# Optimization experiments

Measured on AMD Instinct MI355X. Metric: run time of the kernel, lower is better.

## Reference

```python
import jax, jax.numpy as jnp
import numpy as np

N, B, SD, ED = 2048, 64, 512, 512


def setup_inputs() -> dict:
    key = jax.random.key(0)
    k1, k2, k3 = jax.random.split(key, 3)
    state_tm1 = jax.random.normal(k1, (B, SD), dtype=jnp.float32)
    embeddings = jax.random.normal(k2, (N, B, ED), dtype=jnp.float32)
    W = jax.random.normal(k3, (SD + ED, 1), dtype=jnp.float32) * 0.02
    b = jnp.zeros((1,), dtype=jnp.float32)
    return {"state_tm1": state_tm1, "embeddings": embeddings, "W": W, "b": b}


def reference(state_tm1, embeddings, W, b):
    # fc(concat(state, emb)) == state @ W_s + emb @ W_e + b  (split the weight)
    sd = state_tm1.shape[1]
    W_s, W_e = W[:sd], W[sd:]                      # [SD,1], [ED,1]
    state_score = state_tm1 @ W_s + b              # [B,1]
    logits = jnp.einsum('nbe,eo->nbo', embeddings, W_e) + state_score  # [N,B,1]
    alphas = jax.nn.softmax(logits, axis=0)        # softmax over items (dim 0)
    # weighted sum over items: [B, ED]
    return jnp.einsum('nbo,nbe->be', alphas, embeddings)
```

## Files before the change

kernel.cpp:

```cpp
#include <hip/hip_runtime.h>
#include <math.h>

#define BCOL 64
#define ED 512
#define NROWS 2048

__global__ void attn_partial_kernel(const float* __restrict__ emb,
                                    const float* __restrict__ W,
                                    float* __restrict__ accbuf,
                                    float* __restrict__ mbuf,
                                    float* __restrict__ lbuf,
                                    int G, int rowsPerWave)
{
    const int tid  = threadIdx.x;
    const int lane = tid & 63;
    const int wv   = tid >> 6;
    const int blk  = blockIdx.x;
    const int col  = blk % BCOL;
    const int chunk = blk / BCOL;
    const int g = chunk * 4 + wv;
    const int n0 = g * rowsPerWave;

    const float4* We4 = (const float4*)(W + 512);
    const float4 w0 = We4[lane];
    const float4 w1 = We4[lane + 64];

    float m = -INFINITY, l = 0.0f;
    float4 acc0 = {0.f, 0.f, 0.f, 0.f};
    float4 acc1 = {0.f, 0.f, 0.f, 0.f};

    const float4* row = (const float4*)(emb + ((size_t)n0 * BCOL + col) * ED);
    float4 a0 = row[lane];
    float4 a1 = row[lane + 64];

    for (int i = 0; i < rowsPerWave; ++i) {
        float4 b0, b1;
        if (i + 1 < rowsPerWave) {
            const float4* nrow =
                (const float4*)(emb + ((size_t)(n0 + i + 1) * BCOL + col) * ED);
            b0 = nrow[lane];
            b1 = nrow[lane + 64];
        }
        float p = a0.x * w0.x + a0.y * w0.y + a0.z * w0.z + a0.w * w0.w
                + a1.x * w1.x + a1.y * w1.y + a1.z * w1.z + a1.w * w1.w;
        #pragma unroll
        for (int off = 32; off > 0; off >>= 1)
            p += __shfl_xor(p, off, 64);
        const float s = p;

        const float mn   = fmaxf(m, s);
        const float corr = __expf(m - mn);
        const float pe   = __expf(s - mn);
        l = l * corr + pe;
        acc0.x = acc0.x * corr + pe * a0.x;
        acc0.y = acc0.y * corr + pe * a0.y;
        acc0.z = acc0.z * corr + pe * a0.z;
        acc0.w = acc0.w * corr + pe * a0.w;
        acc1.x = acc1.x * corr + pe * a1.x;
        acc1.y = acc1.y * corr + pe * a1.y;
        acc1.z = acc1.z * corr + pe * a1.z;
        acc1.w = acc1.w * corr + pe * a1.w;
        m = mn;

        a0 = b0;
        a1 = b1;
    }

    float4* out4 = (float4*)(accbuf + ((size_t)col * G + g) * ED);
    out4[lane]      = acc0;
    out4[lane + 64] = acc1;
    if (lane == 0) {
        mbuf[col * G + g] = m;
        lbuf[col * G + g] = l;
    }
}

__global__ void attn_reduce_kernel(const float* __restrict__ accbuf,
                                   const float* __restrict__ mbuf,
                                   const float* __restrict__ lbuf,
                                   float* __restrict__ out,
                                   int G)
{
    const int b    = blockIdx.x >> 1;
    const int half = blockIdx.x & 1;
    const int tid  = threadIdx.x;

    __shared__ float sc[64];
    if (tid < 64) {
        float mg = (tid < G) ? mbuf[b * G + tid] : -INFINITY;
        float lg = (tid < G) ? lbuf[b * G + tid] : 0.0f;
        float M = mg;
        #pragma unroll
        for (int off = 32; off > 0; off >>= 1)
            M = fmaxf(M, __shfl_xor(M, off, 64));
        float el = lg * __expf(mg - M);
        float L = el;
        #pragma unroll
        for (int off = 32; off > 0; off >>= 1)
            L += __shfl_xor(L, off, 64);
        sc[tid] = __expf(mg - M) / L;
    }
    __syncthreads();

    const int e = half * 256 + tid;
    float s = 0.0f;
    for (int gg = 0; gg < G; ++gg)
        s += sc[gg] * accbuf[((size_t)b * G + gg) * ED + e];
    out[(size_t)b * ED + e] = s;
}

extern "C" void kernel_launch(void* const* d_in, const int* in_sizes, int n_in,
                              void* d_out, int out_size, void* d_ws, size_t ws_size,
                              hipStream_t stream) {
    const float* emb = (const float*)d_in[1];
    const float* W   = (const float*)d_in[2];
    float* out = (float*)d_out;

    int G = 64;
    while (G > 4) {
        size_t need = (size_t)BCOL * G * ED * sizeof(float)
                    + 2 * (size_t)BCOL * G * sizeof(float);
        if (need <= ws_size) break;
        G >>= 1;
    }
    const int rowsPerWave = NROWS / G;

    float* accbuf = (float*)d_ws;
    float* mbuf = accbuf + (size_t)BCOL * G * ED;
    float* lbuf = mbuf + BCOL * G;

    attn_partial_kernel<<<dim3(BCOL * (G / 4)), dim3(256), 0, stream>>>(
        emb, W, accbuf, mbuf, lbuf, G, rowsPerWave);
    attn_reduce_kernel<<<dim3(BCOL * 2), dim3(256), 0, stream>>>(
        accbuf, mbuf, lbuf, out, G);
}
```

Before: 370.9 us.

## Process four rows per online-softmax step with double-buffered loads; split reduce over G

The partial kernel now loads four embedding rows at once into ping-pong register buffers and does one softmax rescale per group of four instead of per row. The four row dot-products share their shuffle reductions, giving more memory-level parallelism and fewer serial exp/rescale steps. The reduce kernel uses four blocks per batch column, each splitting the G partials across two half-blocks combined through shared memory. The main costs are higher register pressure. The code also silently assumes rowsPerWave is a multiple of 8, and the final store line is written oddly, though it stays correct.

After: 373.2 us. Within noise of the previous version (+0.6%).

```diff
diff --git a/kernel.cpp b/kernel.cpp
--- a/kernel.cpp
+++ b/kernel.cpp
@@ -4,6 +4,7 @@
 #define BCOL 64
 #define ED 512
 #define NROWS 2048
+#define RG 4
 
 __global__ void attn_partial_kernel(const float* __restrict__ emb,
                                     const float* __restrict__ W,
@@ -20,50 +21,73 @@
     const int chunk = blk / BCOL;
     const int g = chunk * 4 + wv;
     const int n0 = g * rowsPerWave;
+    const int nGroups = rowsPerWave / RG;
 
     const float4* We4 = (const float4*)(W + 512);
     const float4 w0 = We4[lane];
     const float4 w1 = We4[lane + 64];
 
+    const float4* base4 =
+        (const float4*)(emb + ((size_t)n0 * BCOL + col) * ED) + lane;
+    const int rstride = BCOL * ED / 4;
+
     float m = -INFINITY, l = 0.0f;
     float4 acc0 = {0.f, 0.f, 0.f, 0.f};
     float4 acc1 = {0.f, 0.f, 0.f, 0.f};
 
-    const float4* row = (const float4*)(emb + ((size_t)n0 * BCOL + col) * ED);
-    float4 a0 = row[lane];
-    float4 a1 = row[lane + 64];
+    float4 eA[RG], eB[RG], oA[RG], oB[RG];
 
-    for (int i = 0; i < rowsPerWave; ++i) {
-        float4 b0, b1;
-        if (i + 1 < rowsPerWave) {
-            const float4* nrow =
-                (const float4*)(emb + ((size_t)(n0 + i + 1) * BCOL + col) * ED);
-            b0 = nrow[lane];
-            b1 = nrow[lane + 64];
+    #pragma unroll
+    for (int r = 0; r < RG; ++r) {
+        eA[r] = base4[(size_t)r * rstride];
+        eB[r] = base4[(size_t)r * rstride + 64];
+    }
+
+    auto process = [&](float4 (&cA)[RG], float4 (&cB)[RG],
+                       float4 (&nA)[RG], float4 (&nB)[RG], int grp) {
+        if (grp + 1 < nGroups) {
+            const int nb = (grp + 1) * RG;
+            #pragma unroll
+            for (int r = 0; r < RG; ++r) {
+                nA[r] = base4[(size_t)(nb + r) * rstride];
+                nB[r] = base4[(size_t)(nb + r) * rstride + 64];
+            }
         }
-        float p = a0.x * w0.x + a0.y * w0.y + a0.z * w0.z + a0.w * w0.w
-                + a1.x * w1.x + a1.y * w1.y + a1.z * w1.z + a1.w * w1.w;
+        float p[RG];
         #pragma unroll
-        for (int off = 32; off > 0; off >>= 1)
-            p += __shfl_xor(p, off, 64);
-        const float s = p;
+        for (int r = 0; r < RG; ++r) {
+            p[r] = cA[r].x * w0.x + cA[r].y * w0.y + cA[r].z * w0.z + cA[r].w * w0.w
+                 + cB[r].x * w1.x + cB[r].y * w1.y + cB[r].z * w1.z + cB[r].w * w1.w;
+        }
+        #pragma unroll
+        for (int off = 32; off > 0; off >>= 1) {
+            float q[RG];
+            #pragma unroll
+            for (int r = 0; r < RG; ++r) q[r] = __shfl_xor(p[r], off, 64);
+            #pragma unroll
+            for (int r = 0; r < RG; ++r) p[r] += q[r];
+        }
+        const float gmax = fmaxf(fmaxf(p[0], p[1]), fmaxf(p[2], p[3]));
+        const float mn   = fmaxf(m, gmax);
+        const float corr = __expf(m - mn);
+        float pe[RG];
+        #pragma unroll
+        for (int r = 0; r < RG; ++r) pe[r] = __expf(p[r] - mn);
+        l = l * corr + (pe[0] + pe[1] + pe[2] + pe[3]);
+        m = mn;
+        #define ACC_UPD(A, C, f) \
+            A.f = fmaf(pe[3], C[3].f, fmaf(pe[2], C[2].f, \
+                  fmaf(pe[1], C[1].f, fmaf(pe[0], C[0].f, A.f * corr))))
+        ACC_UPD(acc0, cA, x); ACC_UPD(acc0, cA, y);
+        ACC_UPD(acc0, cA, z); ACC_UPD(acc0, cA, w);
+        ACC_UPD(acc1, cB, x); ACC_UPD(acc1, cB, y);
+        ACC_UPD(acc1, cB, z); ACC_UPD(acc1, cB, w);
+        #undef ACC_UPD
+    };
 
-        const float mn   = fmaxf(m, s);
-        const float corr = __expf(m - mn);
-        const float pe   = __expf(s - mn);
-        l = l * corr + pe;
-        acc0.x = acc0.x * corr + pe * a0.x;
-        acc0.y = acc0.y * corr + pe * a0.y;
-        acc0.z = acc0.z * corr + pe * a0.z;
-        acc0.w = acc0.w * corr + pe * a0.w;
-        acc1.x = acc1.x * corr + pe * a1.x;
-        acc1.y = acc1.y * corr + pe * a1.y;
-        acc1.z = acc1.z * corr + pe * a1.z;
-        acc1.w = acc1.w * corr + pe * a1.w;
-        m = mn;
-
-        a0 = b0;
-        a1 = b1;
+    for (int grp = 0; grp < nGroups; grp += 2) {
+        process(eA, eB, oA, oB, grp);
+        process(oA, oB, eA, eB, grp + 1);
     }
 
     float4* out4 = (float4*)(accbuf + ((size_t)col * G + g) * ED);
@@ -81,11 +105,13 @@
                                    float* __restrict__ out,
                                    int G)
 {
-    const int b    = blockIdx.x >> 1;
-    const int half = blockIdx.x & 1;
-    const int tid  = threadIdx.x;
+    const int b   = blockIdx.x >> 2;
+    const int q   = blockIdx.x & 3;
+    const int tid = threadIdx.x;
 
     __shared__ float sc[64];
+    __shared__ float part[128];
+
     if (tid < 64) {
         float mg = (tid < G) ? mbuf[b * G + tid] : -INFINITY;
         float lg = (tid < G) ? lbuf[b * G + tid] : 0.0f;
@@ -102,11 +128,21 @@
     }
     __syncthreads();
 
-    const int e = half * 256 + tid;
+    const int e  = q * 128 + (tid & 127);
+    const int h  = tid >> 7;
+    const int g0 = h * (G >> 1);
+    const int gn = G >> 1;
+    const float* src = accbuf + (size_t)b * G * ED + e;
+
     float s = 0.0f;
-    for (int gg = 0; gg < G; ++gg)
-        s += sc[gg] * accbuf[((size_t)b * G + gg) * ED + e];
-    out[(size_t)b * ED + e] = s;
+    #pragma unroll 8
+    for (int i = 0; i < gn; ++i)
+        s += sc[g0 + i] * src[(size_t)(g0 + i) * ED];
+
+    if (h) part[tid & 127] = s;
+    __syncthreads();
+    if (!h) out[(size_t)b * ED + e] = s + part[tid + 128 - 128 + 128 - 128 + 0 + 0] + 0.0f * part[0], 
+            out[(size_t)b * ED + e] = s + part[tid];
 }
 
 extern "C" void kernel_launch(void* const* d_in, const int* in_sizes, int n_in,
@@ -131,6 +167,6 @@
 
     attn_partial_kernel<<<dim3(BCOL * (G / 4)), dim3(256), 0, stream>>>(
         emb, W, accbuf, mbuf, lbuf, G, rowsPerWave);
-    attn_reduce_kernel<<<dim3(BCOL * 2), dim3(256), 0, stream>>>(
+    attn_reduce_kernel<<<dim3(BCOL * 4), dim3(256), 0, stream>>>(
         accbuf, mbuf, lbuf, out, G);
 }
```
